# Kernel tuning notes

Measured on AMD Instinct MI355X. Metric: run time of the kernel, lower is better.

## Reference

```python
import jax, jax.numpy as jnp
import numpy as np

B, L, D, H, VOCAB = 8, 1024, 1024, 8, 32000
DH = D // H  # dim_per_head = 128
SCALE = float((DH // H) ** (-0.5))  # faithful to key.size(-1)//num_heads
EPS = 1e-5


def setup_inputs() -> dict:
    key = jax.random.key(0)
    ks = jax.random.split(key, 12)
    tokens = jax.random.randint(ks[0], (B, L), 0, VOCAB)
    s = 0.02
    emb = jax.random.normal(ks[1], (VOCAB, D), jnp.float32) * s
    emb = emb.at[0].set(0.0)  # padding_idx=0
    Wq = jax.random.normal(ks[2], (D, D), jnp.float32) * s
    Wk = jax.random.normal(ks[3], (D, D), jnp.float32) * s
    Wv = jax.random.normal(ks[4], (D, D), jnp.float32) * s
    Wo = jax.random.normal(ks[5], (D, D), jnp.float32) * s
    bq = jnp.zeros((D,), jnp.float32)
    bk = jnp.zeros((D,), jnp.float32)
    bv = jnp.zeros((D,), jnp.float32)
    bo = jnp.zeros((D,), jnp.float32)
    gamma = jnp.ones((2 * D,), jnp.float32)
    beta = jnp.zeros((2 * D,), jnp.float32)
    return {"tokens": tokens, "emb": emb, "Wq": Wq, "bq": bq, "Wk": Wk,
            "bk": bk, "Wv": Wv, "bv": bv, "Wo": Wo, "bo": bo,
            "gamma": gamma, "beta": beta}


def reference(tokens, emb, Wq, bq, Wk, bk, Wv, bv, Wo, bo, gamma, beta):
    # padding mask: [B, L, L] True where key token == 0
    pad = (tokens == 0)  # [B, L]
    mask = jnp.broadcast_to(pad[:, None, :], (B, L, L))
    mask = jnp.tile(mask, (H, 1, 1))  # torch .repeat(num_heads,1,1) -> [H*B, L, L]

    x = emb[tokens]  # [B, L, D]

    q = (x @ Wq + bq).reshape(B * H, L, DH)  # faithful interleaved view
    k = (x @ Wk + bk).reshape(B * H, L, DH)
    v = (x @ Wv + bv).reshape(B * H, L, DH)

    scores = jnp.einsum('bqd,bkd->bqk', q, k) * SCALE
    scores = jnp.where(mask, -jnp.inf, scores)
    attn = jax.nn.softmax(scores, axis=-1)
    ctx = jnp.einsum('bqk,bkd->bqd', attn, v).reshape(B, L, D)

    out = ctx @ Wo + bo  # [B, L, D]
    r = x + out
    maxpool = r.max(axis=1)   # [B, D]
    meanpool = r.mean(axis=1)  # [B, D]
    agg = jnp.concatenate([maxpool, meanpool], axis=1)  # [B, 2D]

    mu = agg.mean(axis=-1, keepdims=True)
    var = agg.var(axis=-1, keepdims=True)
    return (agg - mu) / jnp.sqrt(var + EPS) * gamma + beta
```

## Files before the change

### kernel.cpp

```cpp
#include <hip/hip_runtime.h>
#include <math.h>

typedef __attribute__((ext_vector_type(8))) short short8;
typedef __attribute__((ext_vector_type(4))) float f32x4;

constexpr int CB = 8, CL = 1024, CD = 1024, CDH = 128, CM = 8192;
constexpr float CSCALE = 0.25f;
constexpr float CEPS = 1e-5f;

__device__ inline ushort f2b(float f) {
    union { float f; unsigned u; } v; v.f = f;
    unsigned r = v.u + 0x7FFF + ((v.u >> 16) & 1);
    return (ushort)(r >> 16);
}
__device__ inline float b2f(ushort u) {
    union { unsigned u; float f; } v; v.u = ((unsigned)u) << 16;
    return v.f;
}

__device__ inline void gld16(const void* g, void* l) {
    __builtin_amdgcn_global_load_lds(
        (const __attribute__((address_space(1))) void*)g,
        (__attribute__((address_space(3))) void*)l, 16, 0, 0);
}

__global__ __launch_bounds__(256) void k_gather(const int* __restrict__ tokens,
                                                const float* __restrict__ emb,
                                                float* __restrict__ x,
                                                ushort* __restrict__ xb) {
    int row = blockIdx.x;
    int tok = tokens[row];
    float4 v = ((const float4*)(emb + (size_t)tok * CD))[threadIdx.x];
    ((float4*)(x + (size_t)row * CD))[threadIdx.x] = v;
    ushort4 o; o.x = f2b(v.x); o.y = f2b(v.y); o.z = f2b(v.z); o.w = f2b(v.w);
    ((ushort4*)(xb + (size_t)row * CD))[threadIdx.x] = o;
}

__global__ __launch_bounds__(256) void k_wtrans(const float* __restrict__ W0,
                                                const float* __restrict__ W1,
                                                const float* __restrict__ W2,
                                                const float* __restrict__ W3,
                                                ushort* __restrict__ Wt) {
    __shared__ float ws_[32][33];
    const int z = blockIdx.z;
    const float* W = (z == 0) ? W0 : ((z == 1) ? W1 : ((z == 2) ? W2 : W3));
    ushort* Wtz = Wt + (size_t)z * CD * CD;
    const int tk = blockIdx.x * 32, tn = blockIdx.y * 32;
    const int t = threadIdx.x;
    {
        int r = t >> 3, c4 = (t & 7) * 4;
        *(float4*)&ws_[r][c4] = *(const float4*)&W[(size_t)(tk + r) * CD + tn + c4];
    }
    __syncthreads();
    int n = t >> 3, k4 = (t & 7) * 4;
    ushort4 o;
    o.x = f2b(ws_[k4 + 0][n]); o.y = f2b(ws_[k4 + 1][n]);
    o.z = f2b(ws_[k4 + 2][n]); o.w = f2b(ws_[k4 + 3][n]);
    *(ushort4*)&Wtz[(size_t)(tn + n) * CD + tk + k4] = o;
}

__global__ __launch_bounds__(256) void k_gemm_qkv(const ushort* __restrict__ A,
                                                  const ushort* __restrict__ Wt3,
                                                  const float* __restrict__ b0,
                                                  const float* __restrict__ b1,
                                                  const float* __restrict__ b2,
                                                  ushort* __restrict__ C3) {
    __shared__ ushort As[128 * 32];
    __shared__ ushort Bs[128 * 32];
    const int z = blockIdx.z;
    const ushort* Bt  = Wt3 + (size_t)z * CD * CD;
    const float* bias = (z == 0) ? b0 : ((z == 1) ? b1 : b2);
    ushort* Cout      = C3 + (size_t)z * CM * CD;

    const int t = threadIdx.x, w = t >> 6, l = t & 63;
    const int lane15 = l & 15, quad = l >> 4;
    const int bm = (blockIdx.x * 8 + (blockIdx.y >> 3)) * 128;
    const int bn = (blockIdx.y & 7) * 128;
    const int wm = (w >> 1) * 64, wn = (w & 1) * 64;
    const int arow = l >> 2;
    const int aseg = (l & 3) * 8;
    f32x4 acc[4][4] = {};

    for (int k0 = 0; k0 < CD; k0 += 32) {
        __syncthreads();
        #pragma unroll
        for (int c2 = 0; c2 < 2; ++c2) {
            int c = w * 2 + c2;
            gld16(A  + (size_t)(bm + c * 16 + arow) * CD + k0 + aseg, &As[c * 512 + l * 8]);
            gld16(Bt + (size_t)(bn + c * 16 + arow) * CD + k0 + aseg, &Bs[c * 512 + l * 8]);
        }
        __syncthreads();
        short8 af[4], bf[4];
        #pragma unroll
        for (int im = 0; im < 4; ++im)
            af[im] = *(const short8*)&As[(wm + im * 16 + lane15) * 32 + quad * 8];
        #pragma unroll
        for (int in = 0; in < 4; ++in)
            bf[in] = *(const short8*)&Bs[(wn + in * 16 + lane15) * 32 + quad * 8];
        #pragma unroll
        for (int im = 0; im < 4; ++im)
            #pragma unroll
            for (int in = 0; in < 4; ++in)
                acc[im][in] = __builtin_amdgcn_mfma_f32_16x16x32_bf16(af[im], bf[in], acc[im][in], 0, 0, 0);
    }
    #pragma unroll
    for (int in = 0; in < 4; ++in) {
        int col = bn + wn + in * 16 + lane15;
        float bv = bias[col];
        #pragma unroll
        for (int im = 0; im < 4; ++im) {
            int row0 = bm + wm + im * 16 + quad * 4;
            #pragma unroll
            for (int r = 0; r < 4; ++r)
                Cout[(size_t)(row0 + r) * CD + col] = f2b(acc[im][in][r] + bv);
        }
    }
}

__global__ __launch_bounds__(256) void k_gemm_out(const ushort* __restrict__ A,
                                                  const ushort* __restrict__ Bt,
                                                  const float* __restrict__ bias,
                                                  const float* __restrict__ resid,
                                                  float* __restrict__ pmax,
                                                  float* __restrict__ psum) {
    __shared__ ushort As[128 * 32];
    __shared__ ushort Bs[128 * 32];
    __shared__ float redmx[4][64], redsm[4][64];
    const int t = threadIdx.x, w = t >> 6, l = t & 63;
    const int lane15 = l & 15, quad = l >> 4;
    const int bm = (blockIdx.x * 8 + (blockIdx.y >> 3)) * 128;
    const int bn = (blockIdx.y & 7) * 128;
    const int wm = (w >> 1) * 64, wn = (w & 1) * 64;
    const int arow = l >> 2;
    const int aseg = (l & 3) * 8;
    f32x4 acc[4][4] = {};

    for (int k0 = 0; k0 < CD; k0 += 32) {
        __syncthreads();
        #pragma unroll
        for (int c2 = 0; c2 < 2; ++c2) {
            int c = w * 2 + c2;
            gld16(A  + (size_t)(bm + c * 16 + arow) * CD + k0 + aseg, &As[c * 512 + l * 8]);
            gld16(Bt + (size_t)(bn + c * 16 + arow) * CD + k0 + aseg, &Bs[c * 512 + l * 8]);
        }
        __syncthreads();
        short8 af[4], bf[4];
        #pragma unroll
        for (int im = 0; im < 4; ++im)
            af[im] = *(const short8*)&As[(wm + im * 16 + lane15) * 32 + quad * 8];
        #pragma unroll
        for (int in = 0; in < 4; ++in)
            bf[in] = *(const short8*)&Bs[(wn + in * 16 + lane15) * 32 + quad * 8];
        #pragma unroll
        for (int im = 0; im < 4; ++im)
            #pragma unroll
            for (int in = 0; in < 4; ++in)
                acc[im][in] = __builtin_amdgcn_mfma_f32_16x16x32_bf16(af[im], bf[in], acc[im][in], 0, 0, 0);
    }
    const int by = bm >> 7, bb = by >> 3, chunk = by & 7;
    float vmax_[4], vsum_[4];
    #pragma unroll
    for (int in = 0; in < 4; ++in) {
        int col = bn + wn + in * 16 + lane15;
        float bvv = bias[col];
        float mx = -3.4e38f, sm = 0.f;
        #pragma unroll
        for (int im = 0; im < 4; ++im) {
            int row0 = bm + wm + im * 16 + quad * 4;
            #pragma unroll
            for (int r = 0; r < 4; ++r) {
                float rel = acc[im][in][r] + bvv + resid[(size_t)(row0 + r) * CD + col];
                mx = fmaxf(mx, rel);
                sm += rel;
            }
        }
        mx = fmaxf(mx, __shfl_xor(mx, 16));
        mx = fmaxf(mx, __shfl_xor(mx, 32));
        sm += __shfl_xor(sm, 16);
        sm += __shfl_xor(sm, 32);
        vmax_[in] = mx; vsum_[in] = sm;
    }
    if (l < 16) {
        #pragma unroll
        for (int in = 0; in < 4; ++in) {
            redmx[w][in * 16 + lane15] = vmax_[in];
            redsm[w][in * 16 + lane15] = vsum_[in];
        }
    }
    __syncthreads();
    if (t < 128) {
        int wcol = t >> 6, cc = t & 63;
        float m = fmaxf(redmx[wcol][cc], redmx[wcol + 2][cc]);
        float s = redsm[wcol][cc] + redsm[wcol + 2][cc];
        size_t off2 = ((size_t)bb * 8 + chunk) * CD + bn + wcol * 64 + cc;
        pmax[off2] = m;
        psum[off2] = s;
    }
}

__global__ __launch_bounds__(256) void k_vtransp(const ushort* __restrict__ v,
                                                 ushort* __restrict__ Vtp) {
    __shared__ ushort Vs[64 * 136];
    const int i = blockIdx.x >> 4, kt = blockIdx.x & 15;
    const ushort* src = v + (size_t)i * 131072 + (size_t)kt * 64 * 128;
    const int t = threadIdx.x;
    #pragma unroll
    for (int ii = 0; ii < 4; ++ii) {
        int idx = t + 256 * ii;
        int key = idx >> 4, seg = idx & 15;
        *(uint4*)&Vs[key * 136 + seg * 8] = *(const uint4*)&src[key * 128 + seg * 8];
    }
    __syncthreads();
    ushort* dst = Vtp + (size_t)blockIdx.x * 8192;
    #pragma unroll
    for (int it = 0; it < 4; ++it) {
        int L = t + 256 * it;
        int cell = L & 63;
        int quadk = cell >> 4, l15 = cell & 15;
        int p = L >> 6;
        int d = (p >> 1) * 16 + l15;
        int kb = ((p & 1) * 4 + quadk) * 8;
        uint pk[4];
        #pragma unroll
        for (int jj = 0; jj < 4; ++jj) {
            uint lo = Vs[(kb + 2 * jj) * 136 + d];
            uint hi = Vs[(kb + 2 * jj + 1) * 136 + d];
            pk[jj] = lo | (hi << 16);
        }
        *(uint4*)&dst[(size_t)L * 8] = *(uint4*)pk;
    }
}

__device__ inline void attn_stage(const ushort* __restrict__ K,
                                  const ushort* __restrict__ Vtp,
                                  ushort* KsBuf, ushort* VsBuf,
                                  int i, int kt, int w, int l,
                                  int lane15, int quad) {
    #pragma unroll
    for (int c = 0; c < 4; ++c) {
        int p = w * 4 + c;
        gld16(K + (size_t)i * 131072 + (size_t)(kt * 64 + (p >> 2) * 16 + lane15) * 128
                + (p & 3) * 32 + quad * 8,
              KsBuf + p * 512 + (size_t)l * 8);
        gld16(Vtp + ((size_t)(i * 16 + kt) * 16 + p) * 512 + (size_t)l * 8,
              VsBuf + p * 512 + (size_t)l * 8);
    }
}

__global__ __launch_bounds__(256) void k_attn(const ushort* __restrict__ Q,
                                              const ushort* __restrict__ K,
                                              const ushort* __restrict__ Vtp,
                                              const int* __restrict__ tokens,
                                              ushort* __restrict__ ctx) {
    __shared__ ushort Ks[2][16 * 512];
    __shared__ ushort Vs[2][16 * 512];
    __shared__ ushort Ps[4 * 1088];
    __shared__ ushort Msk[CL];
    const int i = blockIdx.x, qb = blockIdx.y * 128;
    const int t = threadIdx.x, w = t >> 6, l = t & 63;
    const int lane15 = l & 15, quad = l >> 4;

    {
        const int* tokb = tokens + (i & 7) * CL;
        #pragma unroll
        for (int jj = 0; jj < 4; ++jj) {
            int idx = t + 256 * jj;
            Msk[idx] = (tokb[idx] == 0) ? (ushort)0xFF80 : (ushort)0;
        }
    }
    short8 af[2][4];
    #pragma unroll
    for (int g = 0; g < 2; ++g)
        #pragma unroll
        for (int kc = 0; kc < 4; ++kc)
            af[g][kc] = *(const short8*)&Q[(size_t)i * 131072
                + (size_t)(qb + w * 32 + g * 16 + lane15) * 128 + kc * 32 + quad * 8];

    f32x4 oacc[2][8];
    #pragma unroll
    for (int g = 0; g < 2; ++g)
        #pragma unroll
        for (int dt = 0; dt < 8; ++dt) oacc[g][dt] = f32x4{0.f, 0.f, 0.f, 0.f};
    float lsum[2][4] = {};
    const int wbase = w * 1088;

    attn_stage(K, Vtp, Ks[0], Vs[0], i, 0, w, l, lane15, quad);
    __syncthreads();

    for (int kt = 0; kt < 16; ++kt) {
        const int cur = kt & 1;
        if (kt < 15)
            attn_stage(K, Vtp, Ks[cur ^ 1], Vs[cur ^ 1], i, kt + 1, w, l, lane15, quad);

        f32x4 sc[2][4];
        __builtin_amdgcn_s_setprio(1);
        #pragma unroll
        for (int j = 0; j < 4; ++j) {
            short8 bk[4];
            #pragma unroll
            for (int kc = 0; kc < 4; ++kc)
                bk[kc] = *(const short8*)&Ks[cur][(j * 4 + kc) * 512 + l * 8];
            #pragma unroll
            for (int g = 0; g < 2; ++g) {
                sc[g][j] = f32x4{0.f, 0.f, 0.f, 0.f};
                #pragma unroll
                for (int kc = 0; kc < 4; ++kc)
                    sc[g][j] = __builtin_amdgcn_mfma_f32_16x16x32_bf16(af[g][kc], bk[kc], sc[g][j], 0, 0, 0);
            }
        }
        __builtin_amdgcn_s_setprio(0);
        #pragma unroll
        for (int j = 0; j < 4; ++j) {
            float mj = b2f(Msk[kt * 64 + j * 16 + lane15]);
            #pragma unroll
            for (int g = 0; g < 2; ++g)
                #pragma unroll
                for (int r = 0; r < 4; ++r) {
                    float pv = __expf(fmaf(sc[g][j][r], CSCALE, mj));
                    sc[g][j][r] = pv;
                    lsum[g][r] += pv;
                }
        }
        short8 ap[2][2];
        #pragma unroll
        for (int g = 0; g < 2; ++g) {
            #pragma unroll
            for (int j = 0; j < 4; ++j) {
                int ks2 = j >> 1;
                int qq  = (j & 1) * 2 + (lane15 >> 3);
                int pos = lane15 & 7;
                #pragma unroll
                for (int r = 0; r < 4; ++r) {
                    union { float f; unsigned u; } cv; cv.f = sc[g][j][r];
                    Ps[wbase + ks2 * 544 + qq * 136 + (quad * 4 + r) * 8 + pos] =
                        (ushort)(cv.u >> 16);
                }
            }
            #pragma unroll
            for (int ks2 = 0; ks2 < 2; ++ks2)
                ap[g][ks2] = *(const short8*)&Ps[wbase + ks2 * 544 + quad * 136 + lane15 * 8];
        }
        __builtin_amdgcn_s_setprio(1);
        #pragma unroll
        for (int dt = 0; dt < 8; ++dt)
            #pragma unroll
            for (int ks2 = 0; ks2 < 2; ++ks2) {
                short8 bv = *(const short8*)&Vs[cur][(dt * 2 + ks2) * 512 + l * 8];
                #pragma unroll
                for (int g = 0; g < 2; ++g)
                    oacc[g][dt] = __builtin_amdgcn_mfma_f32_16x16x32_bf16(ap[g][ks2], bv, oacc[g][dt], 0, 0, 0);
            }
        __builtin_amdgcn_s_setprio(0);
        __syncthreads();
    }
    #pragma unroll
    for (int g = 0; g < 2; ++g) {
        float inv[4];
        #pragma unroll
        for (int r = 0; r < 4; ++r) {
            float s = lsum[g][r];
            #pragma unroll
            for (int off = 1; off < 16; off <<= 1) s += __shfl_xor(s, off);
            inv[r] = 1.f / s;
        }
        #pragma unroll
        for (int dt = 0; dt < 8; ++dt)
            #pragma unroll
            for (int r = 0; r < 4; ++r) {
                int q = qb + w * 32 + g * 16 + quad * 4 + r;
                ctx[(size_t)i * 131072 + (size_t)q * 128 + dt * 16 + lane15] =
                    f2b(oacc[g][dt][r] * inv[r]);
            }
    }
}

__global__ __launch_bounds__(1024) void k_pool2(const float* __restrict__ pmax,
                                                const float* __restrict__ psum,
                                                const float* __restrict__ gamma,
                                                const float* __restrict__ beta,
                                                float* __restrict__ out) {
    __shared__ float rs[16], rq[16];
    __shared__ float s_mu, s_inv;
    const int b = blockIdx.x;
    const int d = threadIdx.x;
    float mx = -3.4e38f, sm = 0.f;
    #pragma unroll
    for (int c = 0; c < 8; ++c) {
        size_t off = ((size_t)b * 8 + c) * CD + d;
        mx = fmaxf(mx, pmax[off]);
        sm += psum[off];
    }
    const float a0 = mx;
    const float a1 = sm * (1.0f / 1024.0f);
    float s = a0 + a1;
    float qd = a0 * a0 + a1 * a1;
    #pragma unroll
    for (int off = 32; off > 0; off >>= 1) {
        s  += __shfl_xor(s, off);
        qd += __shfl_xor(qd, off);
    }
    const int wid = d >> 6;
    if ((d & 63) == 0) { rs[wid] = s; rq[wid] = qd; }
    __syncthreads();
    if (d == 0) {
        float S = 0.f, Qm = 0.f;
        for (int ww = 0; ww < 16; ++ww) { S += rs[ww]; Qm += rq[ww]; }
        float mu  = S * (1.0f / 2048.0f);
        float var = Qm * (1.0f / 2048.0f) - mu * mu;
        s_mu = mu; s_inv = 1.0f / sqrtf(var + CEPS);
    }
    __syncthreads();
    const float mu = s_mu, inv = s_inv;
    out[(size_t)b * 2048 + d]        = (a0 - mu) * inv * gamma[d]        + beta[d];
    out[(size_t)b * 2048 + 1024 + d] = (a1 - mu) * inv * gamma[1024 + d] + beta[1024 + d];
}

extern "C" void kernel_launch(void* const* d_in, const int* in_sizes, int n_in,
                              void* d_out, int out_size, void* d_ws, size_t ws_size,
                              hipStream_t stream) {
    const int*   tokens = (const int*)d_in[0];
    const float* emb    = (const float*)d_in[1];
    const float* Wq     = (const float*)d_in[2];
    const float* bq     = (const float*)d_in[3];
    const float* Wk     = (const float*)d_in[4];
    const float* bk     = (const float*)d_in[5];
    const float* Wv     = (const float*)d_in[6];
    const float* bv     = (const float*)d_in[7];
    const float* Wo     = (const float*)d_in[8];
    const float* bo     = (const float*)d_in[9];
    const float* gamma  = (const float*)d_in[10];
    const float* beta   = (const float*)d_in[11];
    float* out = (float*)d_out;

    char* p = (char*)d_ws;
    float*  x   = (float*)p;   p += (size_t)CM * CD * 4;
    ushort* xb  = (ushort*)p;  p += (size_t)CM * CD * 2;
    ushort* wqt = (ushort*)p;  p += (size_t)CD * CD * 2;
    ushort* wkt = (ushort*)p;  p += (size_t)CD * CD * 2;
    ushort* wvt = (ushort*)p;  p += (size_t)CD * CD * 2;
    ushort* wot = (ushort*)p;  p += (size_t)CD * CD * 2;
    ushort* qb_ = (ushort*)p;  p += (size_t)CM * CD * 2;
    ushort* kb_ = (ushort*)p;  p += (size_t)CM * CD * 2;
    ushort* vb_ = (ushort*)p;  p += (size_t)CM * CD * 2;
    ushort* Vtp = (ushort*)p;  p += (size_t)CM * CD * 2;
    float*  pmax = (float*)p;  p += (size_t)CB * 8 * CD * 4;
    float*  psum = (float*)p;  p += (size_t)CB * 8 * CD * 4;
    ushort* ctx = vb_;
    (void)wkt; (void)wvt;

    k_gather<<<CM, 256, 0, stream>>>(tokens, emb, x, xb);

    dim3 wg(32, 32, 4);
    k_wtrans<<<wg, 256, 0, stream>>>(Wq, Wk, Wv, Wo, wqt);

    dim3 gq(CD / 128, CM / 128, 3);
    k_gemm_qkv<<<gq, 256, 0, stream>>>(xb, wqt, bq, bk, bv, qb_);

    k_vtransp<<<64 * 16, 256, 0, stream>>>(vb_, Vtp);

    dim3 ag(64, 8);
    k_attn<<<ag, 256, 0, stream>>>(qb_, kb_, Vtp, tokens, ctx);

    dim3 go(CD / 128, CM / 128);
    k_gemm_out<<<go, 256, 0, stream>>>(ctx, wot, bo, x, pmax, psum);

    k_pool2<<<CB, 1024, 0, stream>>>(pmax, psum, gamma, beta, out);
}
```

Measured before the change: 351.5 us.

## Drop fp32 embedding copy and stream V fragments directly from global in attention

The gather kernel no longer writes a 32 MB fp32 copy of the embeddings. The output GEMM epilogue instead re-gathers the residual rows from emb through tokens cached in shared memory. Separately, the attention kernel stops staging V tiles in LDS and reads the pre-packed V fragments straight from global memory into registers inside the PV MFMA loop. This halves the LDS footprint and staging traffic, but it exposes global-load latency inside the MFMA loop, with no double buffering for V.

```diff
diff --git a/kernel.cpp b/kernel.cpp
--- a/kernel.cpp
+++ b/kernel.cpp
@@ -26,12 +26,10 @@
 
 __global__ __launch_bounds__(256) void k_gather(const int* __restrict__ tokens,
                                                 const float* __restrict__ emb,
-                                                float* __restrict__ x,
                                                 ushort* __restrict__ xb) {
     int row = blockIdx.x;
     int tok = tokens[row];
     float4 v = ((const float4*)(emb + (size_t)tok * CD))[threadIdx.x];
-    ((float4*)(x + (size_t)row * CD))[threadIdx.x] = v;
     ushort4 o; o.x = f2b(v.x); o.y = f2b(v.y); o.z = f2b(v.z); o.w = f2b(v.w);
     ((ushort4*)(xb + (size_t)row * CD))[threadIdx.x] = o;
 }
@@ -120,12 +118,14 @@
 __global__ __launch_bounds__(256) void k_gemm_out(const ushort* __restrict__ A,
                                                   const ushort* __restrict__ Bt,
                                                   const float* __restrict__ bias,
-                                                  const float* __restrict__ resid,
+                                                  const int* __restrict__ tokens,
+                                                  const float* __restrict__ emb,
                                                   float* __restrict__ pmax,
                                                   float* __restrict__ psum) {
     __shared__ ushort As[128 * 32];
     __shared__ ushort Bs[128 * 32];
     __shared__ float redmx[4][64], redsm[4][64];
+    __shared__ int tokL[128];
     const int t = threadIdx.x, w = t >> 6, l = t & 63;
     const int lane15 = l & 15, quad = l >> 4;
     const int bm = (blockIdx.x * 8 + (blockIdx.y >> 3)) * 128;
@@ -133,6 +133,7 @@
     const int wm = (w >> 1) * 64, wn = (w & 1) * 64;
     const int arow = l >> 2;
     const int aseg = (l & 3) * 8;
+    if (t < 128) tokL[t] = tokens[bm + t];
     f32x4 acc[4][4] = {};
 
     for (int k0 = 0; k0 < CD; k0 += 32) {
@@ -166,10 +167,11 @@
         float mx = -3.4e38f, sm = 0.f;
         #pragma unroll
         for (int im = 0; im < 4; ++im) {
-            int row0 = bm + wm + im * 16 + quad * 4;
+            int rl0 = wm + im * 16 + quad * 4;
             #pragma unroll
             for (int r = 0; r < 4; ++r) {
-                float rel = acc[im][in][r] + bvv + resid[(size_t)(row0 + r) * CD + col];
+                float rv = emb[(size_t)tokL[rl0 + r] * CD + col];
+                float rel = acc[im][in][r] + bvv + rv;
                 mx = fmaxf(mx, rel);
                 sm += rel;
             }
@@ -231,19 +233,16 @@
     }
 }
 
-__device__ inline void attn_stage(const ushort* __restrict__ K,
-                                  const ushort* __restrict__ Vtp,
-                                  ushort* KsBuf, ushort* VsBuf,
-                                  int i, int kt, int w, int l,
-                                  int lane15, int quad) {
+__device__ inline void attn_stageK(const ushort* __restrict__ K,
+                                   ushort* KsBuf,
+                                   int i, int kt, int w, int l,
+                                   int lane15, int quad) {
     #pragma unroll
     for (int c = 0; c < 4; ++c) {
         int p = w * 4 + c;
         gld16(K + (size_t)i * 131072 + (size_t)(kt * 64 + (p >> 2) * 16 + lane15) * 128
                 + (p & 3) * 32 + quad * 8,
               KsBuf + p * 512 + (size_t)l * 8);
-        gld16(Vtp + ((size_t)(i * 16 + kt) * 16 + p) * 512 + (size_t)l * 8,
-              VsBuf + p * 512 + (size_t)l * 8);
     }
 }
 
@@ -253,7 +252,6 @@
                                               const int* __restrict__ tokens,
                                               ushort* __restrict__ ctx) {
     __shared__ ushort Ks[2][16 * 512];
-    __shared__ ushort Vs[2][16 * 512];
     __shared__ ushort Ps[4 * 1088];
     __shared__ ushort Msk[CL];
     const int i = blockIdx.x, qb = blockIdx.y * 128;
@@ -283,14 +281,15 @@
         for (int dt = 0; dt < 8; ++dt) oacc[g][dt] = f32x4{0.f, 0.f, 0.f, 0.f};
     float lsum[2][4] = {};
     const int wbase = w * 1088;
-
-    attn_stage(K, Vtp, Ks[0], Vs[0], i, 0, w, l, lane15, quad);
+    const ushort* vtb = Vtp + (size_t)i * 131072 + (size_t)l * 8;
+
+    attn_stageK(K, Ks[0], i, 0, w, l, lane15, quad);
     __syncthreads();
 
     for (int kt = 0; kt < 16; ++kt) {
         const int cur = kt & 1;
         if (kt < 15)
-            attn_stage(K, Vtp, Ks[cur ^ 1], Vs[cur ^ 1], i, kt + 1, w, l, lane15, quad);
+            attn_stageK(K, Ks[cur ^ 1], i, kt + 1, w, l, lane15, quad);
 
         f32x4 sc[2][4];
         __builtin_amdgcn_s_setprio(1);
@@ -340,12 +339,13 @@
             for (int ks2 = 0; ks2 < 2; ++ks2)
                 ap[g][ks2] = *(const short8*)&Ps[wbase + ks2 * 544 + quad * 136 + lane15 * 8];
         }
+        const ushort* vkt = vtb + (size_t)kt * 16 * 512;
         __builtin_amdgcn_s_setprio(1);
         #pragma unroll
         for (int dt = 0; dt < 8; ++dt)
             #pragma unroll
             for (int ks2 = 0; ks2 < 2; ++ks2) {
-                short8 bv = *(const short8*)&Vs[cur][(dt * 2 + ks2) * 512 + l * 8];
+                short8 bv = *(const short8*)(vkt + (dt * 2 + ks2) * 512);
                 #pragma unroll
                 for (int g = 0; g < 2; ++g)
                     oacc[g][dt] = __builtin_amdgcn_mfma_f32_16x16x32_bf16(ap[g][ks2], bv, oacc[g][dt], 0, 0, 0);
@@ -433,7 +433,6 @@
     float* out = (float*)d_out;
 
     char* p = (char*)d_ws;
-    float*  x   = (float*)p;   p += (size_t)CM * CD * 4;
     ushort* xb  = (ushort*)p;  p += (size_t)CM * CD * 2;
     ushort* wqt = (ushort*)p;  p += (size_t)CD * CD * 2;
     ushort* wkt = (ushort*)p;  p += (size_t)CD * CD * 2;
@@ -448,7 +447,7 @@
     ushort* ctx = vb_;
     (void)wkt; (void)wvt;
 
-    k_gather<<<CM, 256, 0, stream>>>(tokens, emb, x, xb);
+    k_gather<<<CM, 256, 0, stream>>>(tokens, emb, xb);
 
     dim3 wg(32, 32, 4);
     k_wtrans<<<wg, 256, 0, stream>>>(Wq, Wk, Wv, Wo, wqt);
@@ -462,7 +461,7 @@
     k_attn<<<ag, 256, 0, stream>>>(qb_, kb_, Vtp, tokens, ctx);
 
     dim3 go(CD / 128, CM / 128);
-    k_gemm_out<<<go, 256, 0, stream>>>(ctx, wot, bo, x, pmax, psum);
+    k_gemm_out<<<go, 256, 0, stream>>>(ctx, wot, bo, tokens, emb, pmax, psum);
 
     k_pool2<<<CB, 1024, 0, stream>>>(pmax, psum, gamma, beta, out);
 }
```

Measured after the change: 361.2 us. +2.8%, slower.
